# Kernel optimization log

Hardware: AMD Instinct MI355X
Metric: run time of the kernel (lower is better)

## Reference

```python
import jax, jax.numpy as jnp
import numpy as np

NEG = -1e30  # log-space 'zero'
BLANK = 0


def setup_inputs() -> dict:
    key = jax.random.key(0)
    k1, k2, k3, k4, k5, k6 = jax.random.split(key, 6)
    B, T, D, V, L = 16, 500, 256, 5000, 50
    encoder_out = jax.random.normal(k1, (B, T, D), dtype=jnp.float32)
    encoder_out_lens = jax.random.randint(k2, (B,), 400, T + 1, dtype=jnp.int32)
    y = jax.random.randint(k3, (B, L), 1, V, dtype=jnp.int32)  # blank=0 excluded
    y_lens = jax.random.randint(k4, (B,), 30, L + 1, dtype=jnp.int32)
    W = jax.random.normal(k5, (V, D), dtype=jnp.float32) * (1.0 / np.sqrt(D))
    b = jax.random.normal(k6, (V,), dtype=jnp.float32) * 0.01
    return {"encoder_out": encoder_out, "encoder_out_lens": encoder_out_lens,
            "y": y, "y_lens": y_lens, "W": W, "b": b}


def _ctc_neg_logp(lp, ext, skip, enc_lens, y_lens):
    # lp: [T,B,V] log-probs; ext: [B,S] extended label seq (blank interleaved)
    T, B, V = lp.shape
    S = ext.shape[1]
    # per-frame log-probs of the extended labels: [T,B,S]
    lp_ext = jnp.take_along_axis(lp, jnp.broadcast_to(ext[None], (T, B, S)), axis=2)

    end_idx = jnp.stack([2 * y_lens, 2 * y_lens - 1], axis=1)  # [B,2]

    def end_of(alpha):
        vals = jnp.take_along_axis(alpha, end_idx, axis=1)  # [B,2]
        return jnp.logaddexp(vals[:, 0], vals[:, 1])

    alpha0 = jnp.full((B, S), NEG, lp.dtype)
    alpha0 = alpha0.at[:, 0].set(lp_ext[0, :, 0])
    alpha0 = alpha0.at[:, 1].set(lp_ext[0, :, 1])

    pad1 = jnp.full((B, 1), NEG, lp.dtype)
    pad2 = jnp.full((B, 2), NEG, lp.dtype)

    def step(alpha, lp_t):
        prev1 = jnp.concatenate([pad1, alpha[:, :-1]], axis=1)
        prev2 = jnp.concatenate([pad2, alpha[:, :-2]], axis=1)
        m = jnp.logaddexp(alpha, prev1)
        m = jnp.logaddexp(m, jnp.where(skip, prev2, NEG))
        new = m + lp_t
        return new, end_of(new)

    _, ends_rest = jax.lax.scan(step, alpha0, lp_ext[1:])  # [T-1,B]
    ends = jnp.concatenate([end_of(alpha0)[None], ends_rest], axis=0)  # [T,B]
    final = jnp.take_along_axis(ends, (enc_lens - 1)[None, :], axis=0)[0]  # [B]
    return -final


def reference(encoder_out, encoder_out_lens, y, y_lens, W, b):
    # dropout is identity here (deterministic/eval reference)
    B = encoder_out.shape[0]
    logits = jnp.einsum('btd,vd->btv', encoder_out, W) + b  # [B,T,V]
    lp = jax.nn.log_softmax(logits, axis=-1)
    lp = jnp.transpose(lp, (1, 0, 2))  # [T,B,V]

    L = y.shape[1]
    S = 2 * L + 1
    ext = jnp.zeros((B, S), dtype=y.dtype).at[:, 1::2].set(y)  # blank-interleaved
    s_idx = jnp.arange(S)
    ext_m2 = jnp.concatenate([jnp.zeros((B, 2), ext.dtype), ext[:, :-2]], axis=1)
    skip = (s_idx[None, :] >= 2) & (ext != ext_m2) & (ext != BLANK)

    neg_logp = _ctc_neg_logp(lp, ext, skip, encoder_out_lens, y_lens)
    loss = jnp.sum(neg_logp) / B  # CTCLoss(reduction='sum') / batch_size
    return loss
```

## Files before the change

kernel.cpp:

```cpp
#include <hip/hip_runtime.h>
#include <hip/hip_bf16.h>

#define NEG (-1e30f)
#define M_ROWS 8000
#define N_COLS 5000
#define K_DIM  256
#define T_LEN  500
#define T_PAD  512
#define B_SZ   16
#define L_LAB  50
#define LDS_STR 72
#define DP_STR  516
#define LOG2E   1.4426950408889634f
#define LN2     0.6931471805599453f

typedef _Float16 half8  __attribute__((ext_vector_type(8)));
typedef _Float16 half4v __attribute__((ext_vector_type(4)));
typedef float    floatx4 __attribute__((ext_vector_type(4)));

__device__ __forceinline__ float fexp2(float x) {
#if defined(__has_builtin)
#if __has_builtin(__builtin_amdgcn_exp2f)
  return __builtin_amdgcn_exp2f(x);
#else
  return __expf(x * LN2);
#endif
#else
  return __expf(x * LN2);
#endif
}
__device__ __forceinline__ float flog2(float x) {
#if defined(__has_builtin)
#if __has_builtin(__builtin_amdgcn_logf)
  return __builtin_amdgcn_logf(x);
#else
  return __logf(x) * LOG2E;
#endif
#else
  return __logf(x) * LOG2E;
#endif
}
__device__ __forceinline__ float wave_shr1(float x, float fill) {
#if defined(__has_builtin)
#if __has_builtin(__builtin_amdgcn_update_dpp)
  int r = __builtin_amdgcn_update_dpp(__float_as_int(fill), __float_as_int(x),
                                      0x138 , 0xf, 0xf, false);
  return __int_as_float(r);
#else
  return __shfl_up(x, 1);
#endif
#else
  return __shfl_up(x, 1);
#endif
}

__global__ void k_f2h2(const float* __restrict__ enc, const float* __restrict__ W,
                       _Float16* __restrict__ ench, _Float16* __restrict__ wh,
                       float* z, float* psum) {
  int i = blockIdx.x * blockDim.x + threadIdx.x;
  if (i == 0) z[0] = 0.0f;
  if (i < M_ROWS) psum[i] = 0.0f;
  if (i < 512000) {
    float4 v = ((const float4*)enc)[i];
    half4v o = {(_Float16)v.x, (_Float16)v.y, (_Float16)v.z, (_Float16)v.w};
    ((half4v*)ench)[i] = o;
  } else {
    int k = i - 512000;
    if (k < 320000) {
      float4 v = ((const float4*)W)[k];
      half4v o = {(_Float16)v.x, (_Float16)v.y, (_Float16)v.z, (_Float16)v.w};
      ((half4v*)wh)[k] = o;
    }
  }
}

__global__ __launch_bounds__(256) void k_gemm_lse(
    const _Float16* __restrict__ A, const _Float16* __restrict__ Bm,
    const float* __restrict__ bias, const int* __restrict__ y,
    float* __restrict__ psum, float* __restrict__ lgT) {
  __shared__ _Float16 As[128 * LDS_STR];
  __shared__ _Float16 Bs[128 * LDS_STR];

  const int tid = threadIdx.x;
  const int lane = tid & 63;
  const int wid = tid >> 6;
  const int wave_m = wid & 1, wave_n = wid >> 1;
  const int l15 = lane & 15, quad = lane >> 4;
  const int m0 = blockIdx.y * 128, n0 = blockIdx.x * 128;

  floatx4 acc[4][4];
  floatx4 zz = {0.f, 0.f, 0.f, 0.f};
  #pragma unroll
  for (int mi = 0; mi < 4; ++mi)
    #pragma unroll
    for (int ni = 0; ni < 4; ++ni) acc[mi][ni] = zz;

  for (int kk = 0; kk < K_DIM; kk += 64) {
    #pragma unroll
    for (int r = 0; r < 4; ++r) {
      int flat = r * 256 + tid;
      int row = flat >> 3, c8 = flat & 7;
      int ga = m0 + row; if (ga > M_ROWS - 1) ga = M_ROWS - 1;
      int4 av = *(const int4*)(A + (size_t)ga * K_DIM + kk + c8 * 8);
      *(int4*)(As + row * LDS_STR + c8 * 8) = av;
      int gb = n0 + row; if (gb > N_COLS - 1) gb = N_COLS - 1;
      int4 bv = *(const int4*)(Bm + (size_t)gb * K_DIM + kk + c8 * 8);
      *(int4*)(Bs + row * LDS_STR + c8 * 8) = bv;
    }
    __syncthreads();
    #pragma unroll
    for (int ko = 0; ko < 64; ko += 32) {
      half8 af[4], bf[4];
      #pragma unroll
      for (int mi = 0; mi < 4; ++mi)
        af[mi] = *(const half8*)(As + (wave_m * 64 + mi * 16 + l15) * LDS_STR + ko + quad * 8);
      #pragma unroll
      for (int ni = 0; ni < 4; ++ni)
        bf[ni] = *(const half8*)(Bs + (wave_n * 64 + ni * 16 + l15) * LDS_STR + ko + quad * 8);
      #pragma unroll
      for (int mi = 0; mi < 4; ++mi)
        #pragma unroll
        for (int ni = 0; ni < 4; ++ni)
          acc[mi][ni] = __builtin_amdgcn_mfma_f32_16x16x32_f16(af[mi], bf[ni], acc[mi][ni], 0, 0, 0);
    }
    __syncthreads();
  }

  float bvv[4]; bool cok[4];
  #pragma unroll
  for (int ni = 0; ni < 4; ++ni) {
    int col = n0 + wave_n * 64 + ni * 16 + l15;
    cok[ni] = (col < N_COLS);
    bvv[ni] = cok[ni] ? bias[col] : 0.f;
  }

  const int nbase = n0 + wave_n * 64;
  const int mbase = m0 + wave_m * 64;
  int b_lo = mbase / T_LEN;
  int b_hi = (mbase + 63) / T_LEN;
  if (b_hi > B_SZ - 1) b_hi = B_SZ - 1;
  for (int b = b_lo; b <= b_hi; ++b) {
    int v_l = 0x40000000;
    if (lane <= 50) v_l = (lane == 0) ? 0 : y[b * L_LAB + lane - 1];
    int dv_l = v_l - nbase;
    unsigned long long mask = __ballot(dv_l >= 0 && dv_l < 64);
    while (mask) {
      int j = (int)__builtin_ctzll(mask);
      mask &= mask - 1;
      int dv = __shfl(dv_l, j);
      int ni = dv >> 4;
      float bb = bvv[0];
      bb = (ni == 1) ? bvv[1] : bb;
      bb = (ni == 2) ? bvv[2] : bb;
      bb = (ni == 3) ? bvv[3] : bb;
      if ((dv & 15) == l15) {
        #pragma unroll
        for (int mi = 0; mi < 4; ++mi) {
          #pragma unroll
          for (int r = 0; r < 4; ++r) {
            float val = acc[mi][0][r];
            val = (ni == 1) ? acc[mi][1][r] : val;
            val = (ni == 2) ? acc[mi][2][r] : val;
            val = (ni == 3) ? acc[mi][3][r] : val;
            int grow = mbase + mi * 16 + quad * 4 + r;
            int t = grow - b * T_LEN;
            if (t >= 0 && t < T_LEN && grow < M_ROWS)
              lgT[((size_t)b * 51 + j) * T_PAD + t] = val + bb;
          }
        }
      }
    }
  }

  #pragma unroll
  for (int mi = 0; mi < 4; ++mi) {
    #pragma unroll
    for (int r = 0; r < 4; ++r) {
      int grow = mbase + mi * 16 + quad * 4 + r;
      float se = 0.f;
      se += cok[0] ? fexp2((acc[mi][0][r] + bvv[0]) * LOG2E) : 0.f;
      se += cok[1] ? fexp2((acc[mi][1][r] + bvv[1]) * LOG2E) : 0.f;
      se += cok[2] ? fexp2((acc[mi][2][r] + bvv[2]) * LOG2E) : 0.f;
      se += cok[3] ? fexp2((acc[mi][3][r] + bvv[3]) * LOG2E) : 0.f;
      #pragma unroll
      for (int d = 1; d < 16; d <<= 1) se += __shfl_xor(se, d);
      if (l15 == 0 && grow < M_ROWS) atomicAdd(&psum[grow], se);
    }
  }
}

__global__ __launch_bounds__(256) void k_dp(
    const float* __restrict__ lgT, const float* __restrict__ psum,
    const int* __restrict__ enc_lens, const int* __restrict__ y,
    const int* __restrict__ y_lens, float* __restrict__ out) {
  __shared__ float sA[51 * DP_STR];
  __shared__ float sRed[5];
  const int b = blockIdx.x, tid = threadIdx.x;
  const int Tb = enc_lens[b], yl = y_lens[b];

  const float* g = lgT + (size_t)b * 51 * T_PAD;
  #pragma unroll
  for (int k = 0; k < 26; ++k) {
    int idx = tid + k * 256;
    if (idx < 51 * 128) {
      int row = idx >> 7, c4 = (idx & 127) << 2;
      float4 v = *(const float4*)(g + (size_t)row * T_PAD + c4);
      float4 s = {v.x * LOG2E, v.y * LOG2E, v.z * LOG2E, v.w * LOG2E};
      *(float4*)(sA + row * DP_STR + c4) = s;
    }
  }

  float sl2 = 0.f;
  for (int t = tid; t < Tb; t += 256) sl2 += flog2(psum[b * T_LEN + t]);
  #pragma unroll
  for (int d = 1; d < 64; d <<= 1) sl2 += __shfl_xor(sl2, d);
  if ((tid & 63) == 0) sRed[1 + (tid >> 6)] = sl2;
  __syncthreads();
  const float slse = LN2 * (sRed[1] + sRed[2] + sRed[3] + sRed[4]);

  if (tid < 64) {
    const int i = tid;
    const int jj = (i + 1 < 50) ? (i + 1) : 50;
    const float* bl = sA;
    const float* ow = sA + jj * DP_STR;
    const bool v0 = (i <= 50), v1 = (i <= 49);
    const bool lane0 = (i == 0);
    const bool skip1 = (i >= 1 && i <= 49) && (y[b * L_LAB + i] != y[b * L_LAB + i - 1]);

    float4 A0 = *(const float4*)(bl + 0),  A1 = *(const float4*)(ow + 0);
    float4 B0 = *(const float4*)(bl + 4),  B1 = *(const float4*)(ow + 4);
    float4 C0 = *(const float4*)(bl + 8),  C1 = *(const float4*)(ow + 8);
    float4 D0 = *(const float4*)(bl + 12), D1 = *(const float4*)(ow + 12);
    const float4 n4 = {NEG, NEG, NEG, NEG};
    if (!v1) { A1 = n4; B1 = n4; C1 = n4; D1 = n4; }

    float a0 = lane0 ? A0.x : NEG;
    float a1 = lane0 ? A1.x : NEG;

    auto step = [&](float l0r, float l1) {
      float l0 = v0 ? l0r : NEG;
      float p1 = wave_shr1(a1, NEG);
      p1 = lane0 ? NEG : p1;
      float th = skip1 ? p1 : NEG;
      float m0 = fmaxf(a0, p1);
      float na0 = m0 + flog2(fexp2(a0 - m0) + fexp2(p1 - m0)) + l0;
      float m1 = fmaxf(fmaxf(a1, a0), th);
      float na1 = m1 + flog2(fexp2(a1 - m1) + fexp2(a0 - m1) + fexp2(th - m1)) + l1;
      a0 = na0; a1 = na1;
    };

    step(A0.y, A1.y);
    step(A0.z, A1.z);
    step(A0.w, A1.w);

    float4 c0 = B0, c1 = B1, n0v = C0, n1v = C1, nn0 = D0, nn1 = D1;
    int t = 4;
    while (t + 4 <= Tb) {
      float4 p0 = *(const float4*)(bl + t + 12);
      float4 p1v = *(const float4*)(ow + t + 12);
      if (!v1) p1v = n4;
      step(c0.x, c1.x);
      step(c0.y, c1.y);
      step(c0.z, c1.z);
      step(c0.w, c1.w);
      c0 = n0v; c1 = n1v; n0v = nn0; n1v = nn1; nn0 = p0; nn1 = p1v;
      t += 4;
    }
    if (t < Tb) { step(c0.x, c1.x); ++t; }
    if (t < Tb) { step(c0.y, c1.y); ++t; }
    if (t < Tb) { step(c0.z, c1.z); ++t; }

    float ea = __shfl(a0, yl);
    float eb = __shfl(a1, yl - 1);
    if (lane0) {
      float m = fmaxf(ea, eb);
      float fin = LN2 * (m + flog2(fexp2(ea - m) + fexp2(eb - m)));
      atomicAdd(out, (slse - fin) * (1.0f / (float)B_SZ));
    }
  }
}

extern "C" void kernel_launch(void* const* d_in, const int* in_sizes, int n_in,
                              void* d_out, int out_size, void* d_ws, size_t ws_size,
                              hipStream_t stream) {
  (void)in_sizes; (void)n_in; (void)out_size; (void)ws_size;
  const float* enc      = (const float*)d_in[0];
  const int*   enc_lens = (const int*)d_in[1];
  const int*   y        = (const int*)d_in[2];
  const int*   y_lens   = (const int*)d_in[3];
  const float* W        = (const float*)d_in[4];
  const float* bias     = (const float*)d_in[5];
  float* out = (float*)d_out;

  char* ws = (char*)d_ws;
  _Float16* ench = (_Float16*)(ws + 0);
  _Float16* wh   = (_Float16*)(ws + 4096000);
  float* psum    = (float*)(ws + 6656000);
  float* lgT     = (float*)(ws + 6688000);

  k_f2h2<<<3250, 256, 0, stream>>>(enc, W, ench, wh, out, psum);
  k_gemm_lse<<<dim3(40, 63), 256, 0, stream>>>(ench, wh, bias, y, psum, lgT);
  k_dp<<<16, 256, 0, stream>>>(lgT, psum, enc_lens, y, y_lens, out);
}
```

Baseline: 185.9 us.

## Fuse fp32-to-fp16 conversion into GEMM tile loads and store label logits as fp16

Removes the separate conversion kernel: the GEMM now reads fp32 encoder and weight data directly and converts to fp16 while filling LDS. psum is zeroed with a memset and out is zeroed inside the GEMM. Label logits are pre-scaled by log2(e) and stored as fp16, which halves the DP kernel's load traffic. In exchange, the GEMM reads twice the global bytes per tile, with each of its 40 column blocks re-reading the fp32 activations, and the fp16 logits lose precision.

```diff
diff --git a/kernel.cpp b/kernel.cpp
--- a/kernel.cpp
+++ b/kernel.cpp
@@ -15,7 +15,6 @@
 #define LN2     0.6931471805599453f
 
 typedef _Float16 half8  __attribute__((ext_vector_type(8)));
-typedef _Float16 half4v __attribute__((ext_vector_type(4)));
 typedef float    floatx4 __attribute__((ext_vector_type(4)));
 
 __device__ __forceinline__ float fexp2(float x) {
@@ -54,30 +53,10 @@
 #endif
 }
 
-__global__ void k_f2h2(const float* __restrict__ enc, const float* __restrict__ W,
-                       _Float16* __restrict__ ench, _Float16* __restrict__ wh,
-                       float* z, float* psum) {
-  int i = blockIdx.x * blockDim.x + threadIdx.x;
-  if (i == 0) z[0] = 0.0f;
-  if (i < M_ROWS) psum[i] = 0.0f;
-  if (i < 512000) {
-    float4 v = ((const float4*)enc)[i];
-    half4v o = {(_Float16)v.x, (_Float16)v.y, (_Float16)v.z, (_Float16)v.w};
-    ((half4v*)ench)[i] = o;
-  } else {
-    int k = i - 512000;
-    if (k < 320000) {
-      float4 v = ((const float4*)W)[k];
-      half4v o = {(_Float16)v.x, (_Float16)v.y, (_Float16)v.z, (_Float16)v.w};
-      ((half4v*)wh)[k] = o;
-    }
-  }
-}
-
 __global__ __launch_bounds__(256) void k_gemm_lse(
-    const _Float16* __restrict__ A, const _Float16* __restrict__ Bm,
+    const float* __restrict__ A32, const float* __restrict__ W32,
     const float* __restrict__ bias, const int* __restrict__ y,
-    float* __restrict__ psum, float* __restrict__ lgT) {
+    float* __restrict__ psum, _Float16* __restrict__ lgT, float* __restrict__ out) {
   __shared__ _Float16 As[128 * LDS_STR];
   __shared__ _Float16 Bs[128 * LDS_STR];
 
@@ -88,6 +67,8 @@
   const int l15 = lane & 15, quad = lane >> 4;
   const int m0 = blockIdx.y * 128, n0 = blockIdx.x * 128;
 
+  if (blockIdx.x == 0 && blockIdx.y == 0 && tid == 0) out[0] = 0.0f;
+
   floatx4 acc[4][4];
   floatx4 zz = {0.f, 0.f, 0.f, 0.f};
   #pragma unroll
@@ -101,11 +82,17 @@
       int flat = r * 256 + tid;
       int row = flat >> 3, c8 = flat & 7;
       int ga = m0 + row; if (ga > M_ROWS - 1) ga = M_ROWS - 1;
-      int4 av = *(const int4*)(A + (size_t)ga * K_DIM + kk + c8 * 8);
-      *(int4*)(As + row * LDS_STR + c8 * 8) = av;
+      const float* pa = A32 + (size_t)ga * K_DIM + kk + c8 * 8;
+      float4 alo = *(const float4*)pa, ahi = *(const float4*)(pa + 4);
+      half8 ah = {(_Float16)alo.x, (_Float16)alo.y, (_Float16)alo.z, (_Float16)alo.w,
+                  (_Float16)ahi.x, (_Float16)ahi.y, (_Float16)ahi.z, (_Float16)ahi.w};
+      *(half8*)(As + row * LDS_STR + c8 * 8) = ah;
       int gb = n0 + row; if (gb > N_COLS - 1) gb = N_COLS - 1;
-      int4 bv = *(const int4*)(Bm + (size_t)gb * K_DIM + kk + c8 * 8);
-      *(int4*)(Bs + row * LDS_STR + c8 * 8) = bv;
+      const float* pb = W32 + (size_t)gb * K_DIM + kk + c8 * 8;
+      float4 blo = *(const float4*)pb, bhi = *(const float4*)(pb + 4);
+      half8 bh = {(_Float16)blo.x, (_Float16)blo.y, (_Float16)blo.z, (_Float16)blo.w,
+                  (_Float16)bhi.x, (_Float16)bhi.y, (_Float16)bhi.z, (_Float16)bhi.w};
+      *(half8*)(Bs + row * LDS_STR + c8 * 8) = bh;
     }
     __syncthreads();
     #pragma unroll
@@ -165,7 +152,7 @@
             int grow = mbase + mi * 16 + quad * 4 + r;
             int t = grow - b * T_LEN;
             if (t >= 0 && t < T_LEN && grow < M_ROWS)
-              lgT[((size_t)b * 51 + j) * T_PAD + t] = val + bb;
+              lgT[((size_t)b * 51 + j) * T_PAD + t] = (_Float16)((val + bb) * LOG2E);
           }
         }
       }
@@ -190,7 +177,7 @@
 }
 
 __global__ __launch_bounds__(256) void k_dp(
-    const float* __restrict__ lgT, const float* __restrict__ psum,
+    const _Float16* __restrict__ lgT, const float* __restrict__ psum,
     const int* __restrict__ enc_lens, const int* __restrict__ y,
     const int* __restrict__ y_lens, float* __restrict__ out) {
   __shared__ float sA[51 * DP_STR];
@@ -198,15 +185,17 @@
   const int b = blockIdx.x, tid = threadIdx.x;
   const int Tb = enc_lens[b], yl = y_lens[b];
 
-  const float* g = lgT + (size_t)b * 51 * T_PAD;
-  #pragma unroll
-  for (int k = 0; k < 26; ++k) {
+  const _Float16* g = lgT + (size_t)b * 51 * T_PAD;
+  #pragma unroll
+  for (int k = 0; k < 13; ++k) {
     int idx = tid + k * 256;
-    if (idx < 51 * 128) {
-      int row = idx >> 7, c4 = (idx & 127) << 2;
-      float4 v = *(const float4*)(g + (size_t)row * T_PAD + c4);
-      float4 s = {v.x * LOG2E, v.y * LOG2E, v.z * LOG2E, v.w * LOG2E};
-      *(float4*)(sA + row * DP_STR + c4) = s;
+    if (idx < 51 * 64) {
+      int row = idx >> 6, c8 = idx & 63;
+      half8 h = *(const half8*)(g + row * T_PAD + c8 * 8);
+      float4 lo = {(float)h[0], (float)h[1], (float)h[2], (float)h[3]};
+      float4 hi = {(float)h[4], (float)h[5], (float)h[6], (float)h[7]};
+      *(float4*)(sA + row * DP_STR + c8 * 8) = lo;
+      *(float4*)(sA + row * DP_STR + c8 * 8 + 4) = hi;
     }
   }
 
@@ -293,12 +282,10 @@
   float* out = (float*)d_out;
 
   char* ws = (char*)d_ws;
-  _Float16* ench = (_Float16*)(ws + 0);
-  _Float16* wh   = (_Float16*)(ws + 4096000);
-  float* psum    = (float*)(ws + 6656000);
-  float* lgT     = (float*)(ws + 6688000);
-
-  k_f2h2<<<3250, 256, 0, stream>>>(enc, W, ench, wh, out, psum);
-  k_gemm_lse<<<dim3(40, 63), 256, 0, stream>>>(ench, wh, bias, y, psum, lgT);
+  _Float16* lgT = (_Float16*)(ws + 0);
+  float* psum   = (float*)(ws + 835584);
+
+  hipMemsetAsync(psum, 0, M_ROWS * sizeof(float), stream);
+  k_gemm_lse<<<dim3(40, 63), 256, 0, stream>>>(enc, W, bias, y, psum, lgT, out);
   k_dp<<<16, 256, 0, stream>>>(lgT, psum, enc_lens, y, y_lens, out);
 }
```

Result: slower. 194.0 us (+4.3%).

## Fuse convert, GEMM-LSE and CTC DP into one persistent kernel with grid barriers

Applied to the files above, without the earlier changes.

Merges the three launches into one persistent kernel of 768 blocks that convert to fp16, loop over GEMM tiles, and run the CTC recursion in 16 blocks, separated by software grid barriers. The DP moves from log-space logaddexp to linear-space double arithmetic: label probabilities are stored as fp16 log2 values relative to blank, exponentiated once into LDS, and the recursion uses plain multiply-adds. The aim is to remove launch gaps and the per-step exp/log cost on the serial critical path. The risks are grid-barrier correctness (it relies on all blocks being co-resident, with a spin timeout), slow fp64 work, fp16 precision loss, and possible overflow or underflow of the linear-space values.

```diff
diff --git a/kernel.cpp b/kernel.cpp
--- a/kernel.cpp
+++ b/kernel.cpp
@@ -10,11 +10,13 @@
 #define B_SZ   16
 #define L_LAB  50
 #define LDS_STR 72
-#define DP_STR  516
-#define LOG2E   1.4426950408889634f
-#define LN2     0.6931471805599453f
+#define NBLK   768
+#define NTILE  2520
+#define LOG2E  1.4426950408889634f
+#define LN2    0.6931471805599453f
 
 typedef _Float16 half8  __attribute__((ext_vector_type(8)));
+typedef _Float16 half4  __attribute__((ext_vector_type(4)));
 typedef _Float16 half4v __attribute__((ext_vector_type(4)));
 typedef float    floatx4 __attribute__((ext_vector_type(4)));
 
@@ -40,12 +42,15 @@
   return __logf(x) * LOG2E;
 #endif
 }
-__device__ __forceinline__ float wave_shr1(float x, float fill) {
+__device__ __forceinline__ double shr1_f64(double x) {
 #if defined(__has_builtin)
 #if __has_builtin(__builtin_amdgcn_update_dpp)
-  int r = __builtin_amdgcn_update_dpp(__float_as_int(fill), __float_as_int(x),
-                                      0x138 , 0xf, 0xf, false);
-  return __int_as_float(r);
+  long long b = __double_as_longlong(x);
+  int lo = (int)(b & 0xffffffffLL);
+  int hi = (int)(((unsigned long long)b) >> 32);
+  lo = __builtin_amdgcn_update_dpp(0, lo, 0x138 , 0xf, 0xf, false);
+  hi = __builtin_amdgcn_update_dpp(0, hi, 0x138 , 0xf, 0xf, false);
+  return __longlong_as_double(((long long)(unsigned)hi << 32) | (unsigned)lo);
 #else
   return __shfl_up(x, 1);
 #endif
@@ -54,228 +59,248 @@
 #endif
 }
 
-__global__ void k_f2h2(const float* __restrict__ enc, const float* __restrict__ W,
-                       _Float16* __restrict__ ench, _Float16* __restrict__ wh,
-                       float* z, float* psum) {
-  int i = blockIdx.x * blockDim.x + threadIdx.x;
-  if (i == 0) z[0] = 0.0f;
-  if (i < M_ROWS) psum[i] = 0.0f;
-  if (i < 512000) {
-    float4 v = ((const float4*)enc)[i];
-    half4v o = {(_Float16)v.x, (_Float16)v.y, (_Float16)v.z, (_Float16)v.w};
-    ((half4v*)ench)[i] = o;
-  } else {
-    int k = i - 512000;
-    if (k < 320000) {
-      float4 v = ((const float4*)W)[k];
-      half4v o = {(_Float16)v.x, (_Float16)v.y, (_Float16)v.z, (_Float16)v.w};
-      ((half4v*)wh)[k] = o;
-    }
+__device__ __forceinline__ void gbar(unsigned int* c) {
+  __syncthreads();
+  if (threadIdx.x == 0) {
+    __threadfence();
+    __hip_atomic_fetch_add(c, 1u, __ATOMIC_ACQ_REL, __HIP_MEMORY_SCOPE_AGENT);
+    int spins = 0;
+    while (__hip_atomic_load(c, __ATOMIC_ACQUIRE, __HIP_MEMORY_SCOPE_AGENT) < NBLK) {
+      __builtin_amdgcn_s_sleep(16);
+      if (++spins > (1 << 17)) break;
+    }
+    __threadfence();
   }
-}
-
-__global__ __launch_bounds__(256) void k_gemm_lse(
-    const _Float16* __restrict__ A, const _Float16* __restrict__ Bm,
+  __syncthreads();
+}
+
+__global__ __launch_bounds__(256, 3) void k_fused(
+    const float* __restrict__ enc, const float* __restrict__ W,
     const float* __restrict__ bias, const int* __restrict__ y,
-    float* __restrict__ psum, float* __restrict__ lgT) {
-  __shared__ _Float16 As[128 * LDS_STR];
-  __shared__ _Float16 Bs[128 * LDS_STR];
-
+    const int* __restrict__ enc_lens, const int* __restrict__ y_lens,
+    _Float16* __restrict__ ench, _Float16* __restrict__ wh,
+    float* __restrict__ psum, _Float16* __restrict__ lgT,
+    unsigned int* __restrict__ ctr, float* __restrict__ out) {
+  __shared__ __align__(16) char smem[51264];
   const int tid = threadIdx.x;
-  const int lane = tid & 63;
-  const int wid = tid >> 6;
-  const int wave_m = wid & 1, wave_n = wid >> 1;
-  const int l15 = lane & 15, quad = lane >> 4;
-  const int m0 = blockIdx.y * 128, n0 = blockIdx.x * 128;
-
-  floatx4 acc[4][4];
-  floatx4 zz = {0.f, 0.f, 0.f, 0.f};
-  #pragma unroll
-  for (int mi = 0; mi < 4; ++mi)
-    #pragma unroll
-    for (int ni = 0; ni < 4; ++ni) acc[mi][ni] = zz;
-
-  for (int kk = 0; kk < K_DIM; kk += 64) {
-    #pragma unroll
-    for (int r = 0; r < 4; ++r) {
-      int flat = r * 256 + tid;
-      int row = flat >> 3, c8 = flat & 7;
-      int ga = m0 + row; if (ga > M_ROWS - 1) ga = M_ROWS - 1;
-      int4 av = *(const int4*)(A + (size_t)ga * K_DIM + kk + c8 * 8);
-      *(int4*)(As + row * LDS_STR + c8 * 8) = av;
-      int gb = n0 + row; if (gb > N_COLS - 1) gb = N_COLS - 1;
-      int4 bv = *(const int4*)(Bm + (size_t)gb * K_DIM + kk + c8 * 8);
-      *(int4*)(Bs + row * LDS_STR + c8 * 8) = bv;
-    }
-    __syncthreads();
-    #pragma unroll
-    for (int ko = 0; ko < 64; ko += 32) {
-      half8 af[4], bf[4];
+  const int bid = blockIdx.x;
+
+  {
+    int gidx = bid * 256 + tid;
+    if (gidx == 0) out[0] = 0.0f;
+    if (gidx < M_ROWS) psum[gidx] = 0.0f;
+    for (int i = gidx; i < 832000; i += NBLK * 256) {
+      if (i < 512000) {
+        float4 v = ((const float4*)enc)[i];
+        half4v o = {(_Float16)v.x, (_Float16)v.y, (_Float16)v.z, (_Float16)v.w};
+        ((half4v*)ench)[i] = o;
+      } else {
+        int k = i - 512000;
+        float4 v = ((const float4*)W)[k];
+        half4v o = {(_Float16)v.x, (_Float16)v.y, (_Float16)v.z, (_Float16)v.w};
+        ((half4v*)wh)[k] = o;
+      }
+    }
+  }
+  gbar(ctr + 0);
+
+  {
+    _Float16* As = (_Float16*)smem;
+    _Float16* Bs = (_Float16*)(smem + 18432);
+    const int lane = tid & 63;
+    const int wid = tid >> 6;
+    const int wave_m = wid & 1, wave_n = wid >> 1;
+    const int l15 = lane & 15, quad = lane >> 4;
+
+    for (int tile = bid; tile < NTILE; tile += NBLK) {
+      const int n0 = (tile % 40) * 128, m0 = (tile / 40) * 128;
+
+      floatx4 acc[4][4];
+      floatx4 zz = {0.f, 0.f, 0.f, 0.f};
       #pragma unroll
       for (int mi = 0; mi < 4; ++mi)
-        af[mi] = *(const half8*)(As + (wave_m * 64 + mi * 16 + l15) * LDS_STR + ko + quad * 8);
+        #pragma unroll
+        for (int ni = 0; ni < 4; ++ni) acc[mi][ni] = zz;
+
+      for (int kk = 0; kk < K_DIM; kk += 64) {
+        #pragma unroll
+        for (int r = 0; r < 4; ++r) {
+          int flat = r * 256 + tid;
+          int row = flat >> 3, c8 = flat & 7;
+          int ga = m0 + row; if (ga > M_ROWS - 1) ga = M_ROWS - 1;
+          int4 av = *(const int4*)(ench + (size_t)ga * K_DIM + kk + c8 * 8);
+          *(int4*)(As + row * LDS_STR + c8 * 8) = av;
+          int gb = n0 + row; if (gb > N_COLS - 1) gb = N_COLS - 1;
+          int4 bv = *(const int4*)(wh + (size_t)gb * K_DIM + kk + c8 * 8);
+          *(int4*)(Bs + row * LDS_STR + c8 * 8) = bv;
+        }
+        __syncthreads();
+        #pragma unroll
+        for (int ko = 0; ko < 64; ko += 32) {
+          half8 af[4], bf[4];
+          #pragma unroll
+          for (int mi = 0; mi < 4; ++mi)
+            af[mi] = *(const half8*)(As + (wave_m * 64 + mi * 16 + l15) * LDS_STR + ko + quad * 8);
+          #pragma unroll
+          for (int ni = 0; ni < 4; ++ni)
+            bf[ni] = *(const half8*)(Bs + (wave_n * 64 + ni * 16 + l15) * LDS_STR + ko + quad * 8);
+          #pragma unroll
+          for (int mi = 0; mi < 4; ++mi)
+            #pragma unroll
+            for (int ni = 0; ni < 4; ++ni)
+              acc[mi][ni] = __builtin_amdgcn_mfma_f32_16x16x32_f16(af[mi], bf[ni], acc[mi][ni], 0, 0, 0);
+        }
+        __syncthreads();
+      }
+
+      float bvv[4]; bool cok[4];
       #pragma unroll
-      for (int ni = 0; ni < 4; ++ni)
-        bf[ni] = *(const half8*)(Bs + (wave_n * 64 + ni * 16 + l15) * LDS_STR + ko + quad * 8);
-      #pragma unroll
-      for (int mi = 0; mi < 4; ++mi)
-        #pragma unroll
-        for (int ni = 0; ni < 4; ++ni)
-          acc[mi][ni] = __builtin_amdgcn_mfma_f32_16x16x32_f16(af[mi], bf[ni], acc[mi][ni], 0, 0, 0);
-    }
-    __syncthreads();
-  }
-
-  float bvv[4]; bool cok[4];
-  #pragma unroll
-  for (int ni = 0; ni < 4; ++ni) {
-    int col = n0 + wave_n * 64 + ni * 16 + l15;
-    cok[ni] = (col < N_COLS);
-    bvv[ni] = cok[ni] ? bias[col] : 0.f;
-  }
-
-  const int nbase = n0 + wave_n * 64;
-  const int mbase = m0 + wave_m * 64;
-  int b_lo = mbase / T_LEN;
-  int b_hi = (mbase + 63) / T_LEN;
-  if (b_hi > B_SZ - 1) b_hi = B_SZ - 1;
-  for (int b = b_lo; b <= b_hi; ++b) {
-    int v_l = 0x40000000;
-    if (lane <= 50) v_l = (lane == 0) ? 0 : y[b * L_LAB + lane - 1];
-    int dv_l = v_l - nbase;
-    unsigned long long mask = __ballot(dv_l >= 0 && dv_l < 64);
-    while (mask) {
-      int j = (int)__builtin_ctzll(mask);
-      mask &= mask - 1;
-      int dv = __shfl(dv_l, j);
-      int ni = dv >> 4;
-      float bb = bvv[0];
-      bb = (ni == 1) ? bvv[1] : bb;
-      bb = (ni == 2) ? bvv[2] : bb;
-      bb = (ni == 3) ? bvv[3] : bb;
-      if ((dv & 15) == l15) {
-        #pragma unroll
-        for (int mi = 0; mi < 4; ++mi) {
-          #pragma unroll
-          for (int r = 0; r < 4; ++r) {
-            float val = acc[mi][0][r];
-            val = (ni == 1) ? acc[mi][1][r] : val;
-            val = (ni == 2) ? acc[mi][2][r] : val;
-            val = (ni == 3) ? acc[mi][3][r] : val;
-            int grow = mbase + mi * 16 + quad * 4 + r;
-            int t = grow - b * T_LEN;
-            if (t >= 0 && t < T_LEN && grow < M_ROWS)
-              lgT[((size_t)b * 51 + j) * T_PAD + t] = val + bb;
+      for (int ni = 0; ni < 4; ++ni) {
+        int col = n0 + wave_n * 64 + ni * 16 + l15;
+        cok[ni] = (col < N_COLS);
+        bvv[ni] = cok[ni] ? bias[col] : 0.f;
+      }
+
+      const int nbase = n0 + wave_n * 64;
+      const int mbase = m0 + wave_m * 64;
+      int b_lo = mbase / T_LEN;
+      int b_hi = (mbase + 63) / T_LEN;
+      if (b_hi > B_SZ - 1) b_hi = B_SZ - 1;
+      for (int b = b_lo; b <= b_hi; ++b) {
+        int v_l = 0x40000000;
+        if (lane <= 50) v_l = (lane == 0) ? 0 : y[b * L_LAB + lane - 1];
+        int dv_l = v_l - nbase;
+        unsigned long long mask = __ballot(dv_l >= 0 && dv_l < 64);
+        while (mask) {
+          int j = (int)__builtin_ctzll(mask);
+          mask &= mask - 1;
+          int dv = __shfl(dv_l, j);
+          int ni = dv >> 4;
+          float bb = bvv[0];
+          bb = (ni == 1) ? bvv[1] : bb;
+          bb = (ni == 2) ? bvv[2] : bb;
+          bb = (ni == 3) ? bvv[3] : bb;
+          if ((dv & 15) == l15) {
+            #pragma unroll
+            for (int mi = 0; mi < 4; ++mi) {
+              #pragma unroll
+              for (int r = 0; r < 4; ++r) {
+                float val = acc[mi][0][r];
+                val = (ni == 1) ? acc[mi][1][r] : val;
+                val = (ni == 2) ? acc[mi][2][r] : val;
+                val = (ni == 3) ? acc[mi][3][r] : val;
+                int grow = mbase + mi * 16 + quad * 4 + r;
+                int t = grow - b * T_LEN;
+                if (t >= 0 && t < T_LEN && grow < M_ROWS)
+                  lgT[((size_t)b * 51 + j) * T_PAD + t] = (_Float16)((val + bb) * LOG2E);
+              }
+            }
           }
         }
       }
+
+      #pragma unroll
+      for (int mi = 0; mi < 4; ++mi) {
+        #pragma unroll
+        for (int r = 0; r < 4; ++r) {
+          int grow = mbase + mi * 16 + quad * 4 + r;
+          float se = 0.f;
+          se += cok[0] ? fexp2((acc[mi][0][r] + bvv[0]) * LOG2E) : 0.f;
+          se += cok[1] ? fexp2((acc[mi][1][r] + bvv[1]) * LOG2E) : 0.f;
+          se += cok[2] ? fexp2((acc[mi][2][r] + bvv[2]) * LOG2E) : 0.f;
+          se += cok[3] ? fexp2((acc[mi][3][r] + bvv[3]) * LOG2E) : 0.f;
+          #pragma unroll
+          for (int d = 1; d < 16; d <<= 1) se += __shfl_xor(se, d);
+          if (l15 == 0 && grow < M_ROWS) atomicAdd(&psum[grow], se);
+        }
+      }
     }
   }
-
-  #pragma unroll
-  for (int mi = 0; mi < 4; ++mi) {
+  gbar(ctr + 1);
+
+  if (bid < B_SZ) {
+    const int b = bid;
+    const int Tb = enc_lens[b], yl = y_lens[b];
+    _Float16* sQ = (_Float16*)smem;
+    float* sRed = (float*)(smem + 51200);
+    const _Float16* g = lgT + (size_t)b * 51 * T_PAD;
+
     #pragma unroll
-    for (int r = 0; r < 4; ++r) {
-      int grow = mbase + mi * 16 + quad * 4 + r;
-      float se = 0.f;
-      se += cok[0] ? fexp2((acc[mi][0][r] + bvv[0]) * LOG2E) : 0.f;
-      se += cok[1] ? fexp2((acc[mi][1][r] + bvv[1]) * LOG2E) : 0.f;
-      se += cok[2] ? fexp2((acc[mi][2][r] + bvv[2]) * LOG2E) : 0.f;
-      se += cok[3] ? fexp2((acc[mi][3][r] + bvv[3]) * LOG2E) : 0.f;
-      #pragma unroll
-      for (int d = 1; d < 16; d <<= 1) se += __shfl_xor(se, d);
-      if (l15 == 0 && grow < M_ROWS) atomicAdd(&psum[grow], se);
-    }
-  }
-}
-
-__global__ __launch_bounds__(256) void k_dp(
-    const float* __restrict__ lgT, const float* __restrict__ psum,
-    const int* __restrict__ enc_lens, const int* __restrict__ y,
-    const int* __restrict__ y_lens, float* __restrict__ out) {
-  __shared__ float sA[51 * DP_STR];
-  __shared__ float sRed[5];
-  const int b = blockIdx.x, tid = threadIdx.x;
-  const int Tb = enc_lens[b], yl = y_lens[b];
-
-  const float* g = lgT + (size_t)b * 51 * T_PAD;
-  #pragma unroll
-  for (int k = 0; k < 26; ++k) {
-    int idx = tid + k * 256;
-    if (idx < 51 * 128) {
-      int row = idx >> 7, c4 = (idx & 127) << 2;
-      float4 v = *(const float4*)(g + (size_t)row * T_PAD + c4);
-      float4 s = {v.x * LOG2E, v.y * LOG2E, v.z * LOG2E, v.w * LOG2E};
-      *(float4*)(sA + row * DP_STR + c4) = s;
-    }
-  }
-
-  float sl2 = 0.f;
-  for (int t = tid; t < Tb; t += 256) sl2 += flog2(psum[b * T_LEN + t]);
-  #pragma unroll
-  for (int d = 1; d < 64; d <<= 1) sl2 += __shfl_xor(sl2, d);
-  if ((tid & 63) == 0) sRed[1 + (tid >> 6)] = sl2;
-  __syncthreads();
-  const float slse = LN2 * (sRed[1] + sRed[2] + sRed[3] + sRed[4]);
-
-  if (tid < 64) {
-    const int i = tid;
-    const int jj = (i + 1 < 50) ? (i + 1) : 50;
-    const float* bl = sA;
-    const float* ow = sA + jj * DP_STR;
-    const bool v0 = (i <= 50), v1 = (i <= 49);
-    const bool lane0 = (i == 0);
-    const bool skip1 = (i >= 1 && i <= 49) && (y[b * L_LAB + i] != y[b * L_LAB + i - 1]);
-
-    float4 A0 = *(const float4*)(bl + 0),  A1 = *(const float4*)(ow + 0);
-    float4 B0 = *(const float4*)(bl + 4),  B1 = *(const float4*)(ow + 4);
-    float4 C0 = *(const float4*)(bl + 8),  C1 = *(const float4*)(ow + 8);
-    float4 D0 = *(const float4*)(bl + 12), D1 = *(const float4*)(ow + 12);
-    const float4 n4 = {NEG, NEG, NEG, NEG};
-    if (!v1) { A1 = n4; B1 = n4; C1 = n4; D1 = n4; }
-
-    float a0 = lane0 ? A0.x : NEG;
-    float a1 = lane0 ? A1.x : NEG;
-
-    auto step = [&](float l0r, float l1) {
-      float l0 = v0 ? l0r : NEG;
-      float p1 = wave_shr1(a1, NEG);
-      p1 = lane0 ? NEG : p1;
-      float th = skip1 ? p1 : NEG;
-      float m0 = fmaxf(a0, p1);
-      float na0 = m0 + flog2(fexp2(a0 - m0) + fexp2(p1 - m0)) + l0;
-      float m1 = fmaxf(fmaxf(a1, a0), th);
-      float na1 = m1 + flog2(fexp2(a1 - m1) + fexp2(a0 - m1) + fexp2(th - m1)) + l1;
-      a0 = na0; a1 = na1;
-    };
-
-    step(A0.y, A1.y);
-    step(A0.z, A1.z);
-    step(A0.w, A1.w);
-
-    float4 c0 = B0, c1 = B1, n0v = C0, n1v = C1, nn0 = D0, nn1 = D1;
-    int t = 4;
-    while (t + 4 <= Tb) {
-      float4 p0 = *(const float4*)(bl + t + 12);
-      float4 p1v = *(const float4*)(ow + t + 12);
-      if (!v1) p1v = n4;
-      step(c0.x, c1.x);
-      step(c0.y, c1.y);
-      step(c0.z, c1.z);
-      step(c0.w, c1.w);
-      c0 = n0v; c1 = n1v; n0v = nn0; n1v = nn1; nn0 = p0; nn1 = p1v;
-      t += 4;
-    }
-    if (t < Tb) { step(c0.x, c1.x); ++t; }
-    if (t < Tb) { step(c0.y, c1.y); ++t; }
-    if (t < Tb) { step(c0.z, c1.z); ++t; }
-
-    float ea = __shfl(a0, yl);
-    float eb = __shfl(a1, yl - 1);
-    if (lane0) {
-      float m = fmaxf(ea, eb);
-      float fin = LN2 * (m + flog2(fexp2(ea - m) + fexp2(eb - m)));
-      atomicAdd(out, (slse - fin) * (1.0f / (float)B_SZ));
+    for (int k = 0; k < 13; ++k) {
+      int idx = tid + k * 256;
+      if (idx < 50 * 64) {
+        int row = idx >> 6, c8 = idx & 63;
+        half8 h = *(const half8*)(g + (size_t)(row + 1) * T_PAD + c8 * 8);
+        half8 hb = *(const half8*)(g + c8 * 8);
+        half8 o;
+        #pragma unroll
+        for (int e = 0; e < 8; ++e)
+          o[e] = (_Float16)fminf(fexp2((float)h[e] - (float)hb[e]), 60000.0f);
+        *(half8*)(sQ + row * T_PAD + c8 * 8) = o;
+      }
+    }
+
+    float sl2 = 0.f;
+    for (int t = tid; t < Tb; t += 256)
+      sl2 += (float)g[t] - flog2(psum[b * T_LEN + t]);
+    #pragma unroll
+    for (int d = 1; d < 64; d <<= 1) sl2 += __shfl_xor(sl2, d);
+    if ((tid & 63) == 0) sRed[1 + (tid >> 6)] = sl2;
+    __syncthreads();
+    const float base2 = sRed[1] + sRed[2] + sRed[3] + sRed[4];
+
+    if (tid < 64) {
+      const int i = tid;
+      const int rw = (i < 50) ? i : 49;
+      const _Float16* ow = sQ + rw * T_PAD;
+      const bool v1 = (i <= 49);
+      const bool lane0 = (i == 0);
+      const bool skip1 = (i >= 1 && i <= 49) && (y[b * L_LAB + i] != y[b * L_LAB + i - 1]);
+
+      auto ld4 = [&](int t) -> double4 {
+        half4 h = *(const half4*)(ow + t);
+        double4 d;
+        if (v1) { d.x = (float)h[0]; d.y = (float)h[1]; d.z = (float)h[2]; d.w = (float)h[3]; }
+        else    { d.x = 0.0; d.y = 0.0; d.z = 0.0; d.w = 0.0; }
+        return d;
+      };
+      double4 qA = ld4(0), qB = ld4(4), qC = ld4(8), qD = ld4(12);
+
+      double a0 = lane0 ? 1.0 : 0.0;
+      double a1 = lane0 ? qA.x : 0.0;
+
+      auto step = [&](double qd) {
+        double p1 = shr1_f64(a1);
+        p1 = lane0 ? 0.0 : p1;
+        double na0 = a0 + p1;
+        double t3 = skip1 ? p1 : 0.0;
+        double na1 = (a1 + a0 + t3) * qd;
+        a0 = na0; a1 = na1;
+      };
+
+      step(qA.y); step(qA.z); step(qA.w);
+      double4 cur = qB, nxt = qC, nn = qD;
+      int t = 4;
+      while (t + 4 <= Tb) {
+        double4 p = ld4(t + 12);
+        step(cur.x); step(cur.y); step(cur.z); step(cur.w);
+        cur = nxt; nxt = nn; nn = p;
+        t += 4;
+      }
+      if (t < Tb) { step(cur.x); ++t; }
+      if (t < Tb) { step(cur.y); ++t; }
+      if (t < Tb) { step(cur.z); ++t; }
+
+      double ea = __shfl(a0, yl);
+      double eb = __shfl(a1, yl - 1);
+      if (lane0) {
+        double s = ea + eb;
+        long long bb = __double_as_longlong(s);
+        int e2 = (int)((bb >> 52) & 2047) - 1023;
+        double mant = __longlong_as_double((bb & 0x000FFFFFFFFFFFFFLL) | 0x3FF0000000000000LL);
+        float l2fin = (float)e2 + flog2((float)mant);
+        atomicAdd(out, -(base2 + l2fin) * LN2 * (1.0f / (float)B_SZ));
+      }
     }
   }
 }
@@ -296,9 +321,10 @@
   _Float16* ench = (_Float16*)(ws + 0);
   _Float16* wh   = (_Float16*)(ws + 4096000);
   float* psum    = (float*)(ws + 6656000);
-  float* lgT     = (float*)(ws + 6688000);
-
-  k_f2h2<<<3250, 256, 0, stream>>>(enc, W, ench, wh, out, psum);
-  k_gemm_lse<<<dim3(40, 63), 256, 0, stream>>>(ench, wh, bias, y, psum, lgT);
-  k_dp<<<16, 256, 0, stream>>>(lgT, psum, enc_lens, y, y_lens, out);
-}
+  _Float16* lgT  = (_Float16*)(ws + 6688000);
+  unsigned int* ctr = (unsigned int*)(ws + 7523584);
+
+  hipMemsetAsync(ctr, 0, 64, stream);
+  k_fused<<<NBLK, 256, 0, stream>>>(enc, W, bias, y, enc_lens, y_lens,
+                                    ench, wh, psum, lgT, ctr, out);
+}
```

After: 333.9 us. 1.8x slower.
